# Performance work log

Hardware: AMD Instinct MI355X
Metric: run time of the kernel (lower is better)

The kernel has to match this reference:

```python
import jax, jax.numpy as jnp
import numpy as np

N_NODES = 100000
N_EDGES = 1250000
IN_CH, HID_CH, OUT_CH = 128, 64, 40


def setup_inputs() -> dict:
    key = jax.random.key(0)
    ks = jax.random.split(key, 8)
    x = jax.random.normal(ks[0], (N_NODES, IN_CH), dtype=jnp.float32)
    edge_index = jax.random.randint(ks[1], (2, N_EDGES), 0, N_NODES, dtype=jnp.int64)
    # Glorot-ish scaled weights
    W1 = jax.random.normal(ks[2], (IN_CH, HID_CH), dtype=jnp.float32) * (1.0 / np.sqrt(IN_CH))
    b1 = jnp.zeros((HID_CH,), dtype=jnp.float32)
    W2 = jax.random.normal(ks[3], (HID_CH, HID_CH), dtype=jnp.float32) * (1.0 / np.sqrt(HID_CH))
    b2 = jnp.zeros((HID_CH,), dtype=jnp.float32)
    W3 = jax.random.normal(ks[4], (HID_CH, OUT_CH), dtype=jnp.float32) * (1.0 / np.sqrt(HID_CH))
    b3 = jnp.zeros((OUT_CH,), dtype=jnp.float32)
    return {"x": x, "edge_index": edge_index, "W1": W1, "b1": b1,
            "W2": W2, "b2": b2, "W3": W3, "b3": b3}


def reference(x, edge_index, W1, b1, W2, b2, W3, b3):
    n = x.shape[0]
    # PyG GCNConv: add self-loops, symmetric deg^-1/2 normalization
    loop = jnp.arange(n, dtype=edge_index.dtype)
    src = jnp.concatenate([edge_index[0], loop])  # [E+N]
    dst = jnp.concatenate([edge_index[1], loop])
    deg = jax.ops.segment_sum(jnp.ones_like(dst, dtype=x.dtype), dst, num_segments=n)
    dinv = jnp.where(deg > 0, jax.lax.rsqrt(deg), 0.0)
    coef = (dinv[src] * dinv[dst])[:, None]  # [E+N, 1]

    def conv(h, W, b):
        h = h @ W                                  # [N, F_out]
        msg = h[src] * coef                        # gather + scale: [E+N, F_out]
        return jax.ops.segment_sum(msg, dst, num_segments=n) + b

    h = jax.nn.relu(conv(x, W1, b1))   # dropout is identity in eval mode
    h = jax.nn.relu(conv(h, W2, b2))
    h = conv(h, W3, b3)
    return jax.nn.log_softmax(h, axis=1)
```

## Files before the change

### kernel.cpp

```cpp
#include <hip/hip_runtime.h>
#include <hip/hip_fp16.h>

#define NN 100000
#define NE 1250000
#define NBIN 512
#define RBIN 196
#define PAD 16
#define CAP 4096
#define EPB 4096
#define EPT 16

__global__ __launch_bounds__(64) void detect_k(const int* __restrict__ e32, int* __restrict__ flag){
    int lane = threadIdx.x;
    int v = e32[2*lane + 1];
    unsigned long long b = __ballot(v != 0);
    if(lane == 0) flag[0] = (b == 0ULL) ? 1 : 0;
}

__device__ __forceinline__ int eidx(const int* __restrict__ e32, int f, int i){
    return f ? e32[2*(size_t)i] : e32[i];
}

__global__ __launch_bounds__(256) void binA_k(const int* __restrict__ e32, const int* __restrict__ flag,
                                              int* __restrict__ binCnt){
    __shared__ int h[NBIN];
    for(int t = threadIdx.x; t < NBIN; t += 256) h[t] = 0;
    __syncthreads();
    int f = flag[0];
    int base = blockIdx.x * 2048;
    #pragma unroll
    for(int k = 0; k < 8; ++k){
        int i = base + k*256 + threadIdx.x;
        if(i < NE){
            int d = eidx(e32, f, NE + i);
            atomicAdd(&h[d / RBIN], 1);
        }
    }
    __syncthreads();
    for(int t = threadIdx.x; t < NBIN; t += 256){
        int v = h[t];
        if(v) atomicAdd(&binCnt[t*PAD], v);
    }
}

__global__ __launch_bounds__(512) void binB_k(const int* __restrict__ binCnt, int* __restrict__ binOff,
                                              int* __restrict__ binCur, int* __restrict__ rp){
    __shared__ int s[NBIN];
    int t = threadIdx.x;
    int v = binCnt[t*PAD];
    s[t] = v; __syncthreads();
    for(int off = 1; off < NBIN; off <<= 1){
        int u = (t >= off) ? s[t - off] : 0;
        __syncthreads();
        s[t] += u;
        __syncthreads();
    }
    int e = s[t] - v;
    binOff[t] = e;
    binCur[t*PAD] = e;
    if(t == NBIN-1){ binOff[NBIN] = NE; rp[NN] = NE; }
}

__global__ __launch_bounds__(256) void binC_k(const int* __restrict__ e32, const int* __restrict__ flag,
                                              int* __restrict__ binCur, int2* __restrict__ bins){
    __shared__ int2 ST[EPB];
    __shared__ int hist[NBIN];
    __shared__ int lstart[NBIN];
    __shared__ int gbase[NBIN];
    __shared__ int cur[NBIN];
    const int t = threadIdx.x;
    const int e0 = blockIdx.x * EPB;
    const int n = min(EPB, NE - e0);
    const int f = flag[0];

    for(int b = t; b < NBIN; b += 256){ hist[b] = 0; cur[b] = 0; }
    __syncthreads();

    int2 ed[EPT];
    #pragma unroll
    for(int k = 0; k < EPT; ++k){
        int i = k*256 + t;
        if(i < n){
            ed[k].x = eidx(e32, f, e0 + i);
            ed[k].y = eidx(e32, f, NE + e0 + i);
            atomicAdd(&hist[ed[k].y / RBIN], 1);
        }
    }
    __syncthreads();

    if(t < 64){
        int b0 = t*8;
        int pre[8]; int run = 0;
        #pragma unroll
        for(int i = 0; i < 8; ++i){ pre[i] = run; run += hist[b0 + i]; }
        int inc = run;
        for(int o = 1; o < 64; o <<= 1){
            int u = __shfl_up(inc, o, 64);
            if(t >= o) inc += u;
        }
        int excl = inc - run;
        #pragma unroll
        for(int i = 0; i < 8; ++i) lstart[b0 + i] = excl + pre[i];
    }
    for(int b = t; b < NBIN; b += 256) gbase[b] = atomicAdd(&binCur[b*PAD], hist[b]);
    __syncthreads();

    #pragma unroll
    for(int k = 0; k < EPT; ++k){
        int i = k*256 + t;
        if(i < n){
            int b = ed[k].y / RBIN;
            int lo = atomicAdd(&cur[b], 1);
            ST[lstart[b] + lo] = ed[k];
        }
    }
    __syncthreads();

    for(int i = t; i < n; i += 256){
        int2 e = ST[i];
        int b = e.y / RBIN;
        bins[gbase[b] + (i - lstart[b])] = e;
    }
}

__global__ __launch_bounds__(256) void binD_k(const int2* __restrict__ bins, const int* __restrict__ binOff,
                                              int* __restrict__ rp, float* __restrict__ dinv,
                                              int* __restrict__ csr_src){
    __shared__ int2 ES[CAP];
    __shared__ int hist[256];
    __shared__ int sc[256];
    __shared__ int cur[256];
    const int b = blockIdx.x;
    const int nbase = b * RBIN;
    if(nbase >= NN) return;
    const int nend = min(nbase + RBIN, NN);
    const int nr = nend - nbase;
    const int off0 = binOff[b];
    const int cnt  = binOff[b+1] - off0;
    const int t = threadIdx.x;
    hist[t] = 0; cur[t] = 0;
    __syncthreads();

    const bool single = (cnt <= CAP);
    for(int c0 = 0; c0 < cnt; c0 += CAP){
        int n = min(CAP, cnt - c0);
        for(int i = t; i < n; i += 256) ES[i] = bins[off0 + c0 + i];
        __syncthreads();
        for(int i = t; i < n; i += 256) atomicAdd(&hist[ES[i].y - nbase], 1);
        __syncthreads();
    }
    int v = hist[t];
    sc[t] = v; __syncthreads();
    for(int off = 1; off < 256; off <<= 1){
        int u = (t >= off) ? sc[t - off] : 0;
        __syncthreads();
        sc[t] += u;
        __syncthreads();
    }
    int excl = sc[t] - v;
    sc[t] = excl;
    if(t < nr){
        rp[nbase + t]   = off0 + excl;
        dinv[nbase + t] = rsqrtf((float)(v + 1));
    }
    __syncthreads();
    for(int c0 = 0; c0 < cnt; c0 += CAP){
        int n = min(CAP, cnt - c0);
        if(!single){
            for(int i = t; i < n; i += 256) ES[i] = bins[off0 + c0 + i];
            __syncthreads();
        }
        for(int i = t; i < n; i += 256){
            int dl = ES[i].y - nbase;
            int p = atomicAdd(&cur[dl], 1);
            csr_src[off0 + sc[dl] + p] = ES[i].x;
        }
        if(!single) __syncthreads();
    }
}

template<int K, int NC, bool RELU>
__global__ __launch_bounds__(256) void gemm_k(const float* __restrict__ A, const float* __restrict__ W,
                                              const float* __restrict__ dinv,
                                              __half* __restrict__ out, int M){
    constexpr int CH = K/4;
    constexpr int CMASK = CH - 1;
    __shared__ float Xs[64*K];
    __shared__ float Ws[K*NC];
    const int tid  = threadIdx.x;
    const int base = blockIdx.x * 64;

    {
        const float4* Wv = (const float4*)W;
        float4* Wsv = (float4*)Ws;
        #pragma unroll 4
        for(int i = tid; i < K*NC/4; i += 256) Wsv[i] = Wv[i];
    }
    {
        const int ch = tid & (CH - 1);
        const int r0 = tid / CH;
        constexpr int RSTEP = 256 / CH;
        #pragma unroll
        for(int r = r0; r < 64; r += RSTEP){
            int row = base + r; if(row >= M) row = M - 1;
            float4 v = *(const float4*)&A[(size_t)row*K + ch*4];
            if(RELU){ v.x=fmaxf(v.x,0.f); v.y=fmaxf(v.y,0.f); v.z=fmaxf(v.z,0.f); v.w=fmaxf(v.w,0.f); }
            int sw = (ch + r) & CMASK;
            *(float4*)&Xs[r*K + sw*4] = v;
        }
    }
    __syncthreads();

    const int tx = tid & 15, ty = tid >> 4;
    const int c0 = tx * 4;
    float acc[4][4] = {};
    if(c0 < NC){
        for(int k4 = 0; k4 < CH; ++k4){
            float4 xs[4];
            #pragma unroll
            for(int i = 0; i < 4; ++i){
                int r = ty*4 + i;
                int sw = (k4 + r) & CMASK;
                xs[i] = *(const float4*)&Xs[r*K + (sw << 2)];
            }
            float4 wsv[4];
            #pragma unroll
            for(int kk = 0; kk < 4; ++kk) wsv[kk] = *(const float4*)&Ws[(k4*4 + kk)*NC + c0];
            #pragma unroll
            for(int kk = 0; kk < 4; ++kk){
                const float* wp = (const float*)&wsv[kk];
                #pragma unroll
                for(int i = 0; i < 4; ++i){
                    float xv = ((const float*)&xs[i])[kk];
                    #pragma unroll
                    for(int j = 0; j < 4; ++j) acc[i][j] += xv * wp[j];
                }
            }
        }
    }
    #pragma unroll
    for(int i = 0; i < 4; ++i){
        int row = base + ty*4 + i;
        if(row < M && c0 < NC){
            float dv = dinv[row];
            __half2 h01 = __floats2half2_rn(acc[i][0]*dv, acc[i][1]*dv);
            __half2 h23 = __floats2half2_rn(acc[i][2]*dv, acc[i][3]*dv);
            __half2* dst = (__half2*)&out[(size_t)row*NC + c0];
            dst[0] = h01;
            dst[1] = h23;
        }
    }
}

template<int F, bool LSM>
__global__ __launch_bounds__(256) void agg_k(const __half* __restrict__ P, const int* __restrict__ rp,
                                             const int* __restrict__ csr_src,
                                             const float* __restrict__ dinv, const float* __restrict__ bias,
                                             float* __restrict__ G){
    constexpr int NQ = F/4;
    constexpr unsigned F2 = F/2;
    const int lane = threadIdx.x & 63;
    const int v = (blockIdx.x*256 + threadIdx.x) >> 6;
    if(v >= NN) return;
    const int g = lane >> 4;
    const int q = lane & 15;
    const bool qa = (q < NQ);
    const unsigned qo = (unsigned)q*2;
    const __half2* __restrict__ P2 = (const __half2*)P;

    const int beg = rp[v], end = rp[v + 1];
    float4 acc = make_float4(0.f, 0.f, 0.f, 0.f);
    if(g == 0 && qa){
        __half2 a = P2[(unsigned)v*F2 + qo], b = P2[(unsigned)v*F2 + qo + 1];
        float2 fa = __half22float2(a), fb = __half22float2(b);
        acc = make_float4(fa.x, fa.y, fb.x, fb.y);
    }

    int j = beg;
    #pragma unroll 1
    for(; j + 16 <= end; j += 16){
        unsigned i0 = (unsigned)csr_src[j + g]     *F2 + qo;
        unsigned i1 = (unsigned)csr_src[j + 4 + g] *F2 + qo;
        unsigned i2 = (unsigned)csr_src[j + 8 + g] *F2 + qo;
        unsigned i3 = (unsigned)csr_src[j + 12 + g]*F2 + qo;
        __half2 a0 = P2[i0], b0 = P2[i0+1];
        __half2 a1 = P2[i1], b1 = P2[i1+1];
        __half2 a2 = P2[i2], b2 = P2[i2+1];
        __half2 a3 = P2[i3], b3 = P2[i3+1];
        __half2 sa = __hadd2(a0, a1), sb = __hadd2(b0, b1);
        __half2 ta = __hadd2(a2, a3), tb = __hadd2(b2, b3);
        float2 f0 = __half22float2(sa), f1 = __half22float2(sb);
        float2 f2 = __half22float2(ta), f3 = __half22float2(tb);
        acc.x += f0.x + f2.x; acc.y += f0.y + f2.y;
        acc.z += f1.x + f3.x; acc.w += f1.y + f3.y;
    }
    if(j + 8 <= end){
        unsigned i0 = (unsigned)csr_src[j + g]    *F2 + qo;
        unsigned i1 = (unsigned)csr_src[j + 4 + g]*F2 + qo;
        __half2 a0 = P2[i0], b0 = P2[i0+1];
        __half2 a1 = P2[i1], b1 = P2[i1+1];
        __half2 sa = __hadd2(a0, a1), sb = __hadd2(b0, b1);
        float2 f0 = __half22float2(sa), f1 = __half22float2(sb);
        acc.x += f0.x; acc.y += f0.y; acc.z += f1.x; acc.w += f1.y;
        j += 8;
    }
    if(j + 4 <= end){
        unsigned i0 = (unsigned)csr_src[j + g]*F2 + qo;
        __half2 a = P2[i0], b = P2[i0+1];
        float2 fa = __half22float2(a), fb = __half22float2(b);
        acc.x += fa.x; acc.y += fa.y; acc.z += fb.x; acc.w += fb.y;
        j += 4;
    }
    const int rem = end - j;
    if(g < rem){
        unsigned i0 = (unsigned)csr_src[j + g]*F2 + qo;
        __half2 a = P2[i0], b = P2[i0+1];
        float2 fa = __half22float2(a), fb = __half22float2(b);
        acc.x += fa.x; acc.y += fa.y; acc.z += fb.x; acc.w += fb.y;
    }

    #pragma unroll
    for(int m = 16; m <= 32; m <<= 1){
        acc.x += __shfl_xor(acc.x, m, 64);
        acc.y += __shfl_xor(acc.y, m, 64);
        acc.z += __shfl_xor(acc.z, m, 64);
        acc.w += __shfl_xor(acc.w, m, 64);
    }

    float4 r;
    const float d = dinv[v];
    if(g == 0 && qa){
        float4 bb = *(const float4*)&bias[q*4];
        r.x = fmaf(acc.x, d, bb.x);
        r.y = fmaf(acc.y, d, bb.y);
        r.z = fmaf(acc.z, d, bb.z);
        r.w = fmaf(acc.w, d, bb.w);
        if(!LSM) *(float4*)&G[(size_t)v*F + q*4] = r;
    }
    if(LSM){
        float lm = (g == 0 && qa) ? fmaxf(fmaxf(r.x, r.y), fmaxf(r.z, r.w)) : -3.402823466e38f;
        #pragma unroll
        for(int m = 1; m <= 8; m <<= 1) lm = fmaxf(lm, __shfl_xor(lm, m, 64));
        float ls = (g == 0 && qa)
                 ? (__expf(r.x - lm) + __expf(r.y - lm) + __expf(r.z - lm) + __expf(r.w - lm)) : 0.0f;
        #pragma unroll
        for(int m = 1; m <= 8; m <<= 1) ls += __shfl_xor(ls, m, 64);
        if(g == 0 && qa){
            float lz = lm + __logf(ls);
            r.x -= lz; r.y -= lz; r.z -= lz; r.w -= lz;
            *(float4*)&G[(size_t)v*F + q*4] = r;
        }
    }
}

extern "C" void kernel_launch(void* const* d_in, const int* in_sizes, int n_in,
                              void* d_out, int out_size, void* d_ws, size_t ws_size,
                              hipStream_t stream){
    const float* x   = (const float*)d_in[0];
    const int*   e32 = (const int*)  d_in[1];
    const float* W1  = (const float*)d_in[2];
    const float* b1  = (const float*)d_in[3];
    const float* W2  = (const float*)d_in[4];
    const float* b2  = (const float*)d_in[5];
    const float* W3  = (const float*)d_in[6];
    const float* b3  = (const float*)d_in[7];
    float* out = (float*)d_out;

    char* ws = (char*)d_ws;
    size_t off = 0;
    auto alloc = [&](size_t bytes) -> void* {
        void* p = ws + off;
        off = (off + bytes + 255) & ~(size_t)255;
        return p;
    };
    int*    rp     = (int*)   alloc((size_t)(NN+1)*4);
    int*    binCnt = (int*)   alloc((size_t)NBIN*PAD*4);
    int*    binOff = (int*)   alloc((size_t)(NBIN+1)*4);
    int*    binCur = (int*)   alloc((size_t)NBIN*PAD*4);
    int*    flag   = (int*)   alloc(256);
    float*  dinv   = (float*) alloc((size_t)NN*4);
    int*    csr_s  = (int*)   alloc((size_t)NE*4);
    __half* ph     = (__half*)alloc((size_t)NN*64*2);
    float*  gA     = (float*) alloc((size_t)NN*64*4);
    float*  gB     = (float*) alloc((size_t)NN*64*4);
    int2*   bins   = (int2*)  gA;

    hipMemsetAsync(binCnt, 0, (size_t)NBIN*PAD*4, stream);
    detect_k<<<1, 64, 0, stream>>>(e32, flag);
    binA_k<<<(NE + 2047)/2048, 256, 0, stream>>>(e32, flag, binCnt);
    binB_k<<<1, 512, 0, stream>>>(binCnt, binOff, binCur, rp);
    binC_k<<<(NE + EPB - 1)/EPB, 256, 0, stream>>>(e32, flag, binCur, bins);
    binD_k<<<NBIN, 256, 0, stream>>>(bins, binOff, rp, dinv, csr_s);

    const int GEMM_GRID = (NN + 63)/64;
    const int AGG_GRID  = (NN*64 + 255)/256;

    gemm_k<128,64,false><<<GEMM_GRID, 256, 0, stream>>>(x,  W1, dinv, ph, NN);
    agg_k<64,false><<<AGG_GRID, 256, 0, stream>>>(ph, rp, csr_s, dinv, b1, gA);
    gemm_k<64,64,true><<<GEMM_GRID, 256, 0, stream>>>(gA, W2, dinv, ph, NN);
    agg_k<64,false><<<AGG_GRID, 256, 0, stream>>>(ph, rp, csr_s, dinv, b2, gB);
    gemm_k<64,40,true><<<GEMM_GRID, 256, 0, stream>>>(gB, W3, dinv, ph, NN);
    agg_k<40,true><<<AGG_GRID, 256, 0, stream>>>(ph, rp, csr_s, dinv, b3, out);
}
```

Baseline: 270.4 us.

## Fold detect/scan kernels into binning, K-tile GEMM, split aggregation across two waves

The separate detect and bin-scan kernels are removed. Each binning block now detects the index format itself, and the bin-count prefix is recomputed locally in binC and binD. The first GEMM is K-tiled to shrink shared memory and raise occupancy. The 64-wide aggregation now uses two wavefronts per node, each handling 32 features with 8 edges in flight. The 40-wide aggregation loop is shortened. Together these cut launch count and latency, at the cost of redundant scans per block and more waves.

```diff
diff --git a/kernel.cpp b/kernel.cpp
--- a/kernel.cpp
+++ b/kernel.cpp
@@ -10,23 +10,39 @@
 #define EPB 4096
 #define EPT 16
 
-__global__ __launch_bounds__(64) void detect_k(const int* __restrict__ e32, int* __restrict__ flag){
-    int lane = threadIdx.x;
-    int v = e32[2*lane + 1];
-    unsigned long long b = __ballot(v != 0);
-    if(lane == 0) flag[0] = (b == 0ULL) ? 1 : 0;
-}
-
 __device__ __forceinline__ int eidx(const int* __restrict__ e32, int f, int i){
     return f ? e32[2*(size_t)i] : e32[i];
 }
 
-__global__ __launch_bounds__(256) void binA_k(const int* __restrict__ e32, const int* __restrict__ flag,
-                                              int* __restrict__ binCnt){
+__device__ __forceinline__ void scan_bins(const int* __restrict__ binCnt, int* __restrict__ boff){
+    if(threadIdx.x < 64){
+        int b0 = threadIdx.x*8;
+        int pre[8]; int run = 0;
+        #pragma unroll
+        for(int i = 0; i < 8; ++i){ pre[i] = run; run += binCnt[(b0+i)*PAD]; }
+        int inc = run;
+        for(int o = 1; o < 64; o <<= 1){
+            int u = __shfl_up(inc, o, 64);
+            if(threadIdx.x >= (unsigned)o) inc += u;
+        }
+        int excl = inc - run;
+        #pragma unroll
+        for(int i = 0; i < 8; ++i) boff[b0+i] = excl + pre[i];
+    }
+    __syncthreads();
+}
+
+__global__ __launch_bounds__(256) void binA_k(const int* __restrict__ e32, int* __restrict__ binCnt){
     __shared__ int h[NBIN];
+    __shared__ int flg;
     for(int t = threadIdx.x; t < NBIN; t += 256) h[t] = 0;
-    __syncthreads();
-    int f = flag[0];
+    if(threadIdx.x < 64){
+        int v = e32[2*threadIdx.x + 1];
+        unsigned long long b = __ballot(v != 0);
+        if(threadIdx.x == 0) flg = (b == 0ULL) ? 1 : 0;
+    }
+    __syncthreads();
+    const int f = flg;
     int base = blockIdx.x * 2048;
     #pragma unroll
     for(int k = 0; k < 8; ++k){
@@ -43,38 +59,28 @@
     }
 }
 
-__global__ __launch_bounds__(512) void binB_k(const int* __restrict__ binCnt, int* __restrict__ binOff,
-                                              int* __restrict__ binCur, int* __restrict__ rp){
-    __shared__ int s[NBIN];
-    int t = threadIdx.x;
-    int v = binCnt[t*PAD];
-    s[t] = v; __syncthreads();
-    for(int off = 1; off < NBIN; off <<= 1){
-        int u = (t >= off) ? s[t - off] : 0;
-        __syncthreads();
-        s[t] += u;
-        __syncthreads();
-    }
-    int e = s[t] - v;
-    binOff[t] = e;
-    binCur[t*PAD] = e;
-    if(t == NBIN-1){ binOff[NBIN] = NE; rp[NN] = NE; }
-}
-
-__global__ __launch_bounds__(256) void binC_k(const int* __restrict__ e32, const int* __restrict__ flag,
+__global__ __launch_bounds__(256) void binC_k(const int* __restrict__ e32, const int* __restrict__ binCnt,
                                               int* __restrict__ binCur, int2* __restrict__ bins){
     __shared__ int2 ST[EPB];
     __shared__ int hist[NBIN];
     __shared__ int lstart[NBIN];
     __shared__ int gbase[NBIN];
     __shared__ int cur[NBIN];
+    __shared__ int boff[NBIN];
+    __shared__ int flg;
     const int t = threadIdx.x;
     const int e0 = blockIdx.x * EPB;
     const int n = min(EPB, NE - e0);
-    const int f = flag[0];
 
     for(int b = t; b < NBIN; b += 256){ hist[b] = 0; cur[b] = 0; }
-    __syncthreads();
+    if(t < 64){
+        int v = e32[2*t + 1];
+        unsigned long long b = __ballot(v != 0);
+        if(t == 0) flg = (b == 0ULL) ? 1 : 0;
+    }
+    __syncthreads();
+    const int f = flg;
+    scan_bins(binCnt, boff);
 
     int2 ed[EPT];
     #pragma unroll
@@ -102,7 +108,7 @@
         #pragma unroll
         for(int i = 0; i < 8; ++i) lstart[b0 + i] = excl + pre[i];
     }
-    for(int b = t; b < NBIN; b += 256) gbase[b] = atomicAdd(&binCur[b*PAD], hist[b]);
+    for(int b = t; b < NBIN; b += 256) gbase[b] = boff[b] + atomicAdd(&binCur[b*PAD], hist[b]);
     __syncthreads();
 
     #pragma unroll
@@ -123,23 +129,26 @@
     }
 }
 
-__global__ __launch_bounds__(256) void binD_k(const int2* __restrict__ bins, const int* __restrict__ binOff,
+__global__ __launch_bounds__(256) void binD_k(const int2* __restrict__ bins, const int* __restrict__ binCnt,
                                               int* __restrict__ rp, float* __restrict__ dinv,
                                               int* __restrict__ csr_src){
     __shared__ int2 ES[CAP];
     __shared__ int hist[256];
     __shared__ int sc[256];
     __shared__ int cur[256];
+    __shared__ int boff[NBIN];
     const int b = blockIdx.x;
+    const int t = threadIdx.x;
+    if(b == NBIN-1 && t == 0) rp[NN] = NE;
     const int nbase = b * RBIN;
     if(nbase >= NN) return;
     const int nend = min(nbase + RBIN, NN);
     const int nr = nend - nbase;
-    const int off0 = binOff[b];
-    const int cnt  = binOff[b+1] - off0;
-    const int t = threadIdx.x;
     hist[t] = 0; cur[t] = 0;
     __syncthreads();
+    scan_bins(binCnt, boff);
+    const int off0 = boff[b];
+    const int cnt  = binCnt[b*PAD];
 
     const bool single = (cnt <= CAP);
     for(int c0 = 0; c0 < cnt; c0 += CAP){
@@ -179,64 +188,66 @@
     }
 }
 
-template<int K, int NC, bool RELU>
+template<int K, int NC, int KT, bool RELU>
 __global__ __launch_bounds__(256) void gemm_k(const float* __restrict__ A, const float* __restrict__ W,
                                               const float* __restrict__ dinv,
                                               __half* __restrict__ out, int M){
-    constexpr int CH = K/4;
-    constexpr int CMASK = CH - 1;
-    __shared__ float Xs[64*K];
-    __shared__ float Ws[K*NC];
+    constexpr int CHT = KT/4;
+    constexpr int CMASK = CHT - 1;
+    __shared__ float Xs[64*KT];
+    __shared__ float Ws[KT*NC];
     const int tid  = threadIdx.x;
     const int base = blockIdx.x * 64;
-
-    {
-        const float4* Wv = (const float4*)W;
-        float4* Wsv = (float4*)Ws;
-        #pragma unroll 4
-        for(int i = tid; i < K*NC/4; i += 256) Wsv[i] = Wv[i];
-    }
-    {
-        const int ch = tid & (CH - 1);
-        const int r0 = tid / CH;
-        constexpr int RSTEP = 256 / CH;
-        #pragma unroll
-        for(int r = r0; r < 64; r += RSTEP){
-            int row = base + r; if(row >= M) row = M - 1;
-            float4 v = *(const float4*)&A[(size_t)row*K + ch*4];
-            if(RELU){ v.x=fmaxf(v.x,0.f); v.y=fmaxf(v.y,0.f); v.z=fmaxf(v.z,0.f); v.w=fmaxf(v.w,0.f); }
-            int sw = (ch + r) & CMASK;
-            *(float4*)&Xs[r*K + sw*4] = v;
-        }
-    }
-    __syncthreads();
-
     const int tx = tid & 15, ty = tid >> 4;
     const int c0 = tx * 4;
     float acc[4][4] = {};
-    if(c0 < NC){
-        for(int k4 = 0; k4 < CH; ++k4){
-            float4 xs[4];
+
+    for(int k0 = 0; k0 < K; k0 += KT){
+        {
+            const float4* Wv = (const float4*)(W + k0*NC);
+            float4* Wsv = (float4*)Ws;
+            for(int i = tid; i < KT*NC/4; i += 256) Wsv[i] = Wv[i];
+        }
+        {
+            const int ch = tid & (CHT - 1);
+            const int r0 = tid / CHT;
+            constexpr int RSTEP = 256 / CHT;
             #pragma unroll
-            for(int i = 0; i < 4; ++i){
-                int r = ty*4 + i;
-                int sw = (k4 + r) & CMASK;
-                xs[i] = *(const float4*)&Xs[r*K + (sw << 2)];
+            for(int r = r0; r < 64; r += RSTEP){
+                int row = base + r; if(row >= M) row = M - 1;
+                float4 v = *(const float4*)&A[(size_t)row*K + k0 + ch*4];
+                if(RELU){ v.x=fmaxf(v.x,0.f); v.y=fmaxf(v.y,0.f); v.z=fmaxf(v.z,0.f); v.w=fmaxf(v.w,0.f); }
+                int sw = (ch + r) & CMASK;
+                *(float4*)&Xs[r*KT + sw*4] = v;
             }
-            float4 wsv[4];
-            #pragma unroll
-            for(int kk = 0; kk < 4; ++kk) wsv[kk] = *(const float4*)&Ws[(k4*4 + kk)*NC + c0];
-            #pragma unroll
-            for(int kk = 0; kk < 4; ++kk){
-                const float* wp = (const float*)&wsv[kk];
+        }
+        __syncthreads();
+
+        if(c0 < NC){
+            for(int k4 = 0; k4 < CHT; ++k4){
+                float4 xs[4];
                 #pragma unroll
                 for(int i = 0; i < 4; ++i){
-                    float xv = ((const float*)&xs[i])[kk];
+                    int r = ty*4 + i;
+                    int sw = (k4 + r) & CMASK;
+                    xs[i] = *(const float4*)&Xs[r*KT + (sw << 2)];
+                }
+                float4 wsv[4];
+                #pragma unroll
+                for(int kk = 0; kk < 4; ++kk) wsv[kk] = *(const float4*)&Ws[(k4*4 + kk)*NC + c0];
+                #pragma unroll
+                for(int kk = 0; kk < 4; ++kk){
+                    const float* wp = (const float*)&wsv[kk];
                     #pragma unroll
-                    for(int j = 0; j < 4; ++j) acc[i][j] += xv * wp[j];
+                    for(int i = 0; i < 4; ++i){
+                        float xv = ((const float*)&xs[i])[kk];
+                        #pragma unroll
+                        for(int j = 0; j < 4; ++j) acc[i][j] += xv * wp[j];
+                    }
                 }
             }
         }
+        __syncthreads();
     }
     #pragma unroll
     for(int i = 0; i < 4; ++i){
@@ -252,13 +263,82 @@
     }
 }
 
-template<int F, bool LSM>
-__global__ __launch_bounds__(256) void agg_k(const __half* __restrict__ P, const int* __restrict__ rp,
-                                             const int* __restrict__ csr_src,
-                                             const float* __restrict__ dinv, const float* __restrict__ bias,
-                                             float* __restrict__ G){
-    constexpr int NQ = F/4;
-    constexpr unsigned F2 = F/2;
+__global__ __launch_bounds__(256) void aggs_k(const __half* __restrict__ P, const int* __restrict__ rp,
+                                              const int* __restrict__ csr_src,
+                                              const float* __restrict__ dinv, const float* __restrict__ bias,
+                                              float* __restrict__ G){
+    const int lane = threadIdx.x & 63;
+    const int idx  = (blockIdx.x*256 + threadIdx.x) >> 6;
+    const int v    = idx >> 1;
+    const int half = idx & 1;
+    if(v >= NN) return;
+    const int g = lane >> 3;
+    const int q = lane & 7;
+    const unsigned qo = (unsigned)(half*8 + q)*2;
+    const __half2* __restrict__ P2 = (const __half2*)P;
+    constexpr unsigned F2 = 32;
+
+    const int beg = rp[v], end = rp[v + 1];
+    float4 acc = make_float4(0.f, 0.f, 0.f, 0.f);
+    if(g == 0){
+        __half2 a = P2[(unsigned)v*F2 + qo], b = P2[(unsigned)v*F2 + qo + 1];
+        float2 fa = __half22float2(a), fb = __half22float2(b);
+        acc = make_float4(fa.x, fa.y, fb.x, fb.y);
+    }
+
+    int j = beg;
+    #pragma unroll 1
+    for(; j + 16 <= end; j += 16){
+        unsigned i0 = (unsigned)csr_src[j + g]    *F2 + qo;
+        unsigned i1 = (unsigned)csr_src[j + 8 + g]*F2 + qo;
+        __half2 a0 = P2[i0], b0 = P2[i0+1];
+        __half2 a1 = P2[i1], b1 = P2[i1+1];
+        __half2 sa = __hadd2(a0, a1), sb = __hadd2(b0, b1);
+        float2 f0 = __half22float2(sa), f1 = __half22float2(sb);
+        acc.x += f0.x; acc.y += f0.y; acc.z += f1.x; acc.w += f1.y;
+    }
+    if(j + 8 <= end){
+        unsigned i0 = (unsigned)csr_src[j + g]*F2 + qo;
+        __half2 a = P2[i0], b = P2[i0+1];
+        float2 fa = __half22float2(a), fb = __half22float2(b);
+        acc.x += fa.x; acc.y += fa.y; acc.z += fb.x; acc.w += fb.y;
+        j += 8;
+    }
+    const int rem = end - j;
+    if(g < rem){
+        unsigned i0 = (unsigned)csr_src[j + g]*F2 + qo;
+        __half2 a = P2[i0], b = P2[i0+1];
+        float2 fa = __half22float2(a), fb = __half22float2(b);
+        acc.x += fa.x; acc.y += fa.y; acc.z += fb.x; acc.w += fb.y;
+    }
+
+    #pragma unroll
+    for(int m = 8; m <= 32; m <<= 1){
+        acc.x += __shfl_xor(acc.x, m, 64);
+        acc.y += __shfl_xor(acc.y, m, 64);
+        acc.z += __shfl_xor(acc.z, m, 64);
+        acc.w += __shfl_xor(acc.w, m, 64);
+    }
+
+    if(g == 0){
+        const float d = dinv[v];
+        float4 bb = *(const float4*)&bias[half*32 + q*4];
+        float4 r;
+        r.x = fmaf(acc.x, d, bb.x);
+        r.y = fmaf(acc.y, d, bb.y);
+        r.z = fmaf(acc.z, d, bb.z);
+        r.w = fmaf(acc.w, d, bb.w);
+        *(float4*)&G[(size_t)v*64 + half*32 + q*4] = r;
+    }
+}
+
+__global__ __launch_bounds__(256) void agg40_k(const __half* __restrict__ P, const int* __restrict__ rp,
+                                               const int* __restrict__ csr_src,
+                                               const float* __restrict__ dinv, const float* __restrict__ bias,
+                                               float* __restrict__ G){
+    constexpr int F = 40;
+    constexpr int NQ = 10;
+    constexpr unsigned F2 = 20;
     const int lane = threadIdx.x & 63;
     const int v = (blockIdx.x*256 + threadIdx.x) >> 6;
     if(v >= NN) return;
@@ -278,23 +358,7 @@
 
     int j = beg;
     #pragma unroll 1
-    for(; j + 16 <= end; j += 16){
-        unsigned i0 = (unsigned)csr_src[j + g]     *F2 + qo;
-        unsigned i1 = (unsigned)csr_src[j + 4 + g] *F2 + qo;
-        unsigned i2 = (unsigned)csr_src[j + 8 + g] *F2 + qo;
-        unsigned i3 = (unsigned)csr_src[j + 12 + g]*F2 + qo;
-        __half2 a0 = P2[i0], b0 = P2[i0+1];
-        __half2 a1 = P2[i1], b1 = P2[i1+1];
-        __half2 a2 = P2[i2], b2 = P2[i2+1];
-        __half2 a3 = P2[i3], b3 = P2[i3+1];
-        __half2 sa = __hadd2(a0, a1), sb = __hadd2(b0, b1);
-        __half2 ta = __hadd2(a2, a3), tb = __hadd2(b2, b3);
-        float2 f0 = __half22float2(sa), f1 = __half22float2(sb);
-        float2 f2 = __half22float2(ta), f3 = __half22float2(tb);
-        acc.x += f0.x + f2.x; acc.y += f0.y + f2.y;
-        acc.z += f1.x + f3.x; acc.w += f1.y + f3.y;
-    }
-    if(j + 8 <= end){
+    for(; j + 8 <= end; j += 8){
         unsigned i0 = (unsigned)csr_src[j + g]    *F2 + qo;
         unsigned i1 = (unsigned)csr_src[j + 4 + g]*F2 + qo;
         __half2 a0 = P2[i0], b0 = P2[i0+1];
@@ -302,7 +366,6 @@
         __half2 sa = __hadd2(a0, a1), sb = __hadd2(b0, b1);
         float2 f0 = __half22float2(sa), f1 = __half22float2(sb);
         acc.x += f0.x; acc.y += f0.y; acc.z += f1.x; acc.w += f1.y;
-        j += 8;
     }
     if(j + 4 <= end){
         unsigned i0 = (unsigned)csr_src[j + g]*F2 + qo;
@@ -335,21 +398,18 @@
         r.y = fmaf(acc.y, d, bb.y);
         r.z = fmaf(acc.z, d, bb.z);
         r.w = fmaf(acc.w, d, bb.w);
-        if(!LSM) *(float4*)&G[(size_t)v*F + q*4] = r;
-    }
-    if(LSM){
-        float lm = (g == 0 && qa) ? fmaxf(fmaxf(r.x, r.y), fmaxf(r.z, r.w)) : -3.402823466e38f;
-        #pragma unroll
-        for(int m = 1; m <= 8; m <<= 1) lm = fmaxf(lm, __shfl_xor(lm, m, 64));
-        float ls = (g == 0 && qa)
-                 ? (__expf(r.x - lm) + __expf(r.y - lm) + __expf(r.z - lm) + __expf(r.w - lm)) : 0.0f;
-        #pragma unroll
-        for(int m = 1; m <= 8; m <<= 1) ls += __shfl_xor(ls, m, 64);
-        if(g == 0 && qa){
-            float lz = lm + __logf(ls);
-            r.x -= lz; r.y -= lz; r.z -= lz; r.w -= lz;
-            *(float4*)&G[(size_t)v*F + q*4] = r;
-        }
+    }
+    float lm = (g == 0 && qa) ? fmaxf(fmaxf(r.x, r.y), fmaxf(r.z, r.w)) : -3.402823466e38f;
+    #pragma unroll
+    for(int m = 1; m <= 8; m <<= 1) lm = fmaxf(lm, __shfl_xor(lm, m, 64));
+    float ls = (g == 0 && qa)
+             ? (__expf(r.x - lm) + __expf(r.y - lm) + __expf(r.z - lm) + __expf(r.w - lm)) : 0.0f;
+    #pragma unroll
+    for(int m = 1; m <= 8; m <<= 1) ls += __shfl_xor(ls, m, 64);
+    if(g == 0 && qa){
+        float lz = lm + __logf(ls);
+        r.x -= lz; r.y -= lz; r.z -= lz; r.w -= lz;
+        *(float4*)&G[(size_t)v*F + q*4] = r;
     }
 }
 
@@ -373,11 +433,9 @@
         off = (off + bytes + 255) & ~(size_t)255;
         return p;
     };
+    int*    binCnt = (int*)   alloc((size_t)NBIN*PAD*4);
+    int*    binCur = (int*)   alloc((size_t)NBIN*PAD*4);
     int*    rp     = (int*)   alloc((size_t)(NN+1)*4);
-    int*    binCnt = (int*)   alloc((size_t)NBIN*PAD*4);
-    int*    binOff = (int*)   alloc((size_t)(NBIN+1)*4);
-    int*    binCur = (int*)   alloc((size_t)NBIN*PAD*4);
-    int*    flag   = (int*)   alloc(256);
     float*  dinv   = (float*) alloc((size_t)NN*4);
     int*    csr_s  = (int*)   alloc((size_t)NE*4);
     __half* ph     = (__half*)alloc((size_t)NN*64*2);
@@ -385,20 +443,19 @@
     float*  gB     = (float*) alloc((size_t)NN*64*4);
     int2*   bins   = (int2*)  gA;
 
-    hipMemsetAsync(binCnt, 0, (size_t)NBIN*PAD*4, stream);
-    detect_k<<<1, 64, 0, stream>>>(e32, flag);
-    binA_k<<<(NE + 2047)/2048, 256, 0, stream>>>(e32, flag, binCnt);
-    binB_k<<<1, 512, 0, stream>>>(binCnt, binOff, binCur, rp);
-    binC_k<<<(NE + EPB - 1)/EPB, 256, 0, stream>>>(e32, flag, binCur, bins);
-    binD_k<<<NBIN, 256, 0, stream>>>(bins, binOff, rp, dinv, csr_s);
+    hipMemsetAsync(binCnt, 0, (size_t)2*NBIN*PAD*4, stream);
+    binA_k<<<(NE + 2047)/2048, 256, 0, stream>>>(e32, binCnt);
+    binC_k<<<(NE + EPB - 1)/EPB, 256, 0, stream>>>(e32, binCnt, binCur, bins);
+    binD_k<<<NBIN, 256, 0, stream>>>(bins, binCnt, rp, dinv, csr_s);
 
     const int GEMM_GRID = (NN + 63)/64;
+    const int AGGS_GRID = NN/2;
     const int AGG_GRID  = (NN*64 + 255)/256;
 
-    gemm_k<128,64,false><<<GEMM_GRID, 256, 0, stream>>>(x,  W1, dinv, ph, NN);
-    agg_k<64,false><<<AGG_GRID, 256, 0, stream>>>(ph, rp, csr_s, dinv, b1, gA);
-    gemm_k<64,64,true><<<GEMM_GRID, 256, 0, stream>>>(gA, W2, dinv, ph, NN);
-    agg_k<64,false><<<AGG_GRID, 256, 0, stream>>>(ph, rp, csr_s, dinv, b2, gB);
-    gemm_k<64,40,true><<<GEMM_GRID, 256, 0, stream>>>(gB, W3, dinv, ph, NN);
-    agg_k<40,true><<<AGG_GRID, 256, 0, stream>>>(ph, rp, csr_s, dinv, b3, out);
-}
+    gemm_k<128,64,64,false><<<GEMM_GRID, 256, 0, stream>>>(x,  W1, dinv, ph, NN);
+    aggs_k<<<AGGS_GRID, 256, 0, stream>>>(ph, rp, csr_s, dinv, b1, gA);
+    gemm_k<64,64,64,true><<<GEMM_GRID, 256, 0, stream>>>(gA, W2, dinv, ph, NN);
+    aggs_k<<<AGGS_GRID, 256, 0, stream>>>(ph, rp, csr_s, dinv, b2, gB);
+    gemm_k<64,40,64,true><<<GEMM_GRID, 256, 0, stream>>>(gB, W3, dinv, ph, NN);
+    agg40_k<<<AGG_GRID, 256, 0, stream>>>(ph, rp, csr_s, dinv, b3, out);
+}
```

After: 305.2 us. +12.9%, slower.
